# Optimization experiments

Measured on AMD Instinct MI355X. Metric: run time of the kernel, lower is better.

## Reference

```python
import jax, jax.numpy as jnp
import numpy as np

B, T, D, H = 4, 1024, 256, 4
DK = D // H


def setup_inputs() -> dict:
    key = jax.random.key(0)
    ks = jax.random.split(key, 5)
    scale = 1.0 / np.sqrt(D)
    return {
        "x": jax.random.normal(ks[0], (B, T, D), dtype=jnp.float32),
        "Wqkv": jax.random.normal(ks[1], (3 * D, D), dtype=jnp.float32) * scale,
        "bqkv": jax.random.normal(ks[2], (3 * D,), dtype=jnp.float32) * 0.01,
        "Wproj": jax.random.normal(ks[3], (D, D), dtype=jnp.float32) * scale,
        "bproj": jax.random.normal(ks[4], (D,), dtype=jnp.float32) * 0.01,
    }


def reference(x, Wqkv, bqkv, Wproj, bproj):
    # ---- temporal multi-head self-attention over T ----
    qkv = x @ Wqkv.T + bqkv                      # (B,T,3D)
    q, k, v = jnp.split(qkv, 3, axis=-1)         # each (B,T,D)
    def split_heads(t):
        return t.reshape(B, T, H, DK).transpose(0, 2, 1, 3)  # (B,H,T,DK)
    q, k, v = split_heads(q), split_heads(k), split_heads(v)
    scores_t = jnp.einsum('bhtd,bhsd->bhts', q, k) / jnp.sqrt(jnp.float32(DK))
    w_t = jax.nn.softmax(scores_t, axis=-1)       # (B,H,T,T)
    ctx = jnp.einsum('bhts,bhsd->bhtd', w_t, v)   # (B,H,T,DK)
    ctx = ctx.transpose(0, 2, 1, 3).reshape(B, T, D)
    y_t = ctx @ Wproj.T + bproj                   # (B,T,D)

    # ---- spatial (feature-pairwise) attention per timestep ----
    scores_f = jnp.einsum('bti,btj->btij', x, x) / jnp.sqrt(jnp.float32(D))  # (B,T,F,F)
    w_f = jax.nn.softmax(scores_f, axis=-1)
    y_f = jnp.einsum('btij,btj->bti', w_f, x)     # (B,T,D)

    # serial mode: y = y_t + y_f
    return y_t + y_f
```

## Files before the change

kernel.cpp:

```cpp
#include <hip/hip_runtime.h>
#include <hip/hip_bf16.h>


typedef __attribute__((ext_vector_type(8))) short short8;
typedef __attribute__((ext_vector_type(4))) float f32x4;

__device__ __forceinline__ short f2bf(float f) {
    __hip_bfloat16 h = __float2bfloat16(f);
    return __builtin_bit_cast(short, h);
}
__device__ __forceinline__ float b2f(short s) {
    unsigned u = ((unsigned)(unsigned short)s) << 16;
    return __builtin_bit_cast(float, u);
}
__device__ __forceinline__ short8 pack8(float4 a, float4 b) {
    return (short8){ f2bf(a.x), f2bf(a.y), f2bf(a.z), f2bf(a.w),
                     f2bf(b.x), f2bf(b.y), f2bf(b.z), f2bf(b.w) };
}

#if __has_builtin(__builtin_amdgcn_exp2f)
__device__ __forceinline__ float fast_exp2(float f) { return __builtin_amdgcn_exp2f(f); }
#else
__device__ __forceinline__ float fast_exp2(float f) { return exp2f(f); }
#endif

__global__ __launch_bounds__(256) void k_qkv_sp(
    const float* __restrict__ x,
    const float* __restrict__ wq,
    const float* __restrict__ bqkv,
    short* __restrict__ qkvb,
    short* __restrict__ vT,
    float* __restrict__ yf)
{
    const int bx = blockIdx.x;
    const int tid = threadIdx.x;

    if (bx >= 768) {
        const int w = tid >> 6, lane = tid & 63;
        const int row = (bx - 768)*4 + w;
        const float* xr = &x[(size_t)row*256];
        float xj[4], u[4];
        #pragma unroll
        for (int q = 0; q < 4; ++q) { xj[q] = xr[lane + q*64]; u[q] = xj[q] * 0.25f; }
        float S[16];
        float t0 = 1.f, t1 = 1.f, t2 = 1.f, t3 = 1.f;
        #pragma unroll
        for (int k = 0; k < 16; ++k) {
            S[k] = (t0 + t1) + (t2 + t3);
            if (k < 15) { t0 *= u[0]; t1 *= u[1]; t2 *= u[2]; t3 *= u[3]; }
        }
        #pragma unroll
        for (int k = 0; k < 16; ++k) {
            #pragma unroll
            for (int off = 32; off >= 1; off >>= 1)
                S[k] += __shfl_xor(S[k], off);
        }
        const float invfact[16] = {
            1.f, 1.f, 0.5f, 1.f/6, 1.f/24, 1.f/120, 1.f/720, 1.f/5040,
            1.f/40320, 1.f/362880, 1.f/3628800, 1.f/39916800, 1.f/479001600,
            1.f/6227020800.f, 1.f/87178291200.f, 1.f/1307674368000.f };
        float a[16], bcf[15];
        #pragma unroll
        for (int k = 0; k < 16; ++k) a[k] = S[k] * invfact[k];
        #pragma unroll
        for (int k = 0; k < 15; ++k) bcf[k] = 4.f * S[k+1] * invfact[k];
        float* yr = &yf[(size_t)row*256];
        #pragma unroll
        for (int q = 0; q < 4; ++q) {
            float v = u[q];
            float den = a[15];
            #pragma unroll
            for (int k = 14; k >= 0; --k) den = fmaf(den, v, a[k]);
            float num = bcf[14];
            #pragma unroll
            for (int k = 13; k >= 0; --k) num = fmaf(num, v, bcf[k]);
            yr[lane + q*64] = num / den;
        }
        return;
    }

    __shared__ __attribute__((aligned(16))) short As[64*64];
    __shared__ __attribute__((aligned(16))) short Bs[64*64];
    const int bn = bx >> 6, bm = bx & 63;
    const int w = tid >> 6, lane = tid & 63, ln = lane & 15, quad = lane >> 4;
    const int r0 = tid >> 3, c0 = (tid & 7) * 8;

    float4 xa0, xa1, xb0, xb1, wa0, wa1, wb0, wb1;
#define LOADT(K0) { \
    const float* pa0 = &x[(size_t)(bm*64 + r0)*256 + (K0) + c0]; \
    xa0 = *(const float4*)pa0; xa1 = *(const float4*)(pa0 + 4); \
    const float* pa1 = &x[(size_t)(bm*64 + r0 + 32)*256 + (K0) + c0]; \
    xb0 = *(const float4*)pa1; xb1 = *(const float4*)(pa1 + 4); \
    const float* pw0 = &wq[(size_t)(bn*64 + r0)*256 + (K0) + c0]; \
    wa0 = *(const float4*)pw0; wa1 = *(const float4*)(pw0 + 4); \
    const float* pw1 = &wq[(size_t)(bn*64 + r0 + 32)*256 + (K0) + c0]; \
    wb0 = *(const float4*)pw1; wb1 = *(const float4*)(pw1 + 4); }

    f32x4 acc[4];
    #pragma unroll
    for (int i = 0; i < 4; ++i) acc[i] = (f32x4){0.f,0.f,0.f,0.f};

    LOADT(0);
    for (int k0 = 0; k0 < 256; k0 += 64) {
        *(short8*)&As[r0*64 + c0]      = pack8(xa0, xa1);
        *(short8*)&As[(r0+32)*64 + c0] = pack8(xb0, xb1);
        *(short8*)&Bs[r0*64 + c0]      = pack8(wa0, wa1);
        *(short8*)&Bs[(r0+32)*64 + c0] = pack8(wb0, wb1);
        __syncthreads();
        if (k0 < 192) LOADT(k0 + 64);
        #pragma unroll
        for (int ks = 0; ks < 2; ++ks) {
            short8 bf = *(const short8*)&Bs[(w*16 + ln)*64 + ks*32 + quad*8];
            #pragma unroll
            for (int mt = 0; mt < 4; ++mt) {
                short8 af = *(const short8*)&As[(mt*16 + ln)*64 + ks*32 + quad*8];
                acc[mt] = __builtin_amdgcn_mfma_f32_16x16x32_bf16(af, bf, acc[mt], 0, 0, 0);
            }
        }
        if (k0 < 192) __syncthreads();
    }
#undef LOADT
    const int n = bn*64 + w*16 + ln;
    const float bias = bqkv[n];
    #pragma unroll
    for (int mt = 0; mt < 4; ++mt) {
        #pragma unroll
        for (int r = 0; r < 4; ++r) {
            int m = bm*64 + mt*16 + quad*4 + r;
            float v = acc[mt][r] + bias;
            if (bn < 8) qkvb[(size_t)m*512 + n] = f2bf(v);
            else        vT[(size_t)(n - 512)*4096 + m] = f2bf(v);
        }
    }
}

__global__ __launch_bounds__(256) void k_attn(
    const short* __restrict__ qkvb,
    const short* __restrict__ vT,
    short* __restrict__ opart,
    float* __restrict__ lpart)
{
    __shared__ __attribute__((aligned(16))) char smem[27648];
    short* Ks = (short*)smem;
    short* Vs = (short*)(smem + 9216);
    short* Ps = (short*)(smem + 18432);
    const int bx = blockIdx.x;
    const int tid = threadIdx.x;
    const int w = tid >> 6, lane = tid & 63;
    const int qb = bx >> 2, quarter = bx & 3;
    const int h = blockIdx.y, b = blockIdx.z;
    const int ln = lane & 15, quad = lane >> 4;
    const int qg = b*1024 + qb*64 + w*16 + ln;
    const float SC = 0.18033688f;

    short8 qf[2];
    #pragma unroll
    for (int ks = 0; ks < 2; ++ks)
        qf[ks] = *(const short8*)&qkvb[(size_t)qg*512 + h*64 + ks*32 + quad*8];

    const int sr0 = tid >> 3, sc0 = (tid & 7) * 8;
    const int sr1 = sr0 + 32;
    short8 kreg[2], vreg[2];
#define LOADC(CH) { \
    kreg[0] = *(const short8*)&qkvb[(size_t)(b*1024 + (CH)*64 + sr0)*512 + 256 + h*64 + sc0]; \
    vreg[0] = *(const short8*)&vT[(size_t)(h*64 + sr0)*4096 + b*1024 + (CH)*64 + sc0]; \
    kreg[1] = *(const short8*)&qkvb[(size_t)(b*1024 + (CH)*64 + sr1)*512 + 256 + h*64 + sc0]; \
    vreg[1] = *(const short8*)&vT[(size_t)(h*64 + sr1)*4096 + b*1024 + (CH)*64 + sc0]; }

    f32x4 O[4];
    #pragma unroll
    for (int i = 0; i < 4; ++i) O[i] = (f32x4){0.f,0.f,0.f,0.f};
    float lrow[4] = {0.f, 0.f, 0.f, 0.f};

    const int cbase = quarter*4;
    LOADC(cbase);
    for (int kc = 0; kc < 4; ++kc) {
        __syncthreads();
        *(short8*)&Ks[sr0*72 + sc0] = kreg[0];
        *(short8*)&Vs[sr0*72 + sc0] = vreg[0];
        *(short8*)&Ks[sr1*72 + sc0] = kreg[1];
        *(short8*)&Vs[sr1*72 + sc0] = vreg[1];
        __syncthreads();
        if (kc < 3) LOADC(cbase + kc + 1);

        f32x4 s[4];
        #pragma unroll
        for (int nt = 0; nt < 4; ++nt) {
            s[nt] = (f32x4){0.f,0.f,0.f,0.f};
            #pragma unroll
            for (int ks = 0; ks < 2; ++ks) {
                short8 kf = *(const short8*)&Ks[(nt*16 + ln)*72 + ks*32 + quad*8];
                s[nt] = __builtin_amdgcn_mfma_f32_16x16x32_bf16(qf[ks], kf, s[nt], 0, 0, 0);
            }
        }
        #pragma unroll
        for (int nt = 0; nt < 4; ++nt) {
            #pragma unroll
            for (int r = 0; r < 4; ++r) {
                float e = fast_exp2(s[nt][r] * SC);
                lrow[r] += e;
                Ps[w*1152 + (quad*4 + r)*72 + nt*16 + ln] = f2bf(e);
            }
        }
        short8 pf[2];
        #pragma unroll
        for (int ks = 0; ks < 2; ++ks)
            pf[ks] = *(const short8*)&Ps[w*1152 + ln*72 + ks*32 + quad*8];

        #pragma unroll
        for (int dt = 0; dt < 4; ++dt) {
            #pragma unroll
            for (int ks = 0; ks < 2; ++ks) {
                short8 vf = *(const short8*)&Vs[(dt*16 + ln)*72 + ks*32 + quad*8];
                O[dt] = __builtin_amdgcn_mfma_f32_16x16x32_bf16(pf[ks], vf, O[dt], 0, 0, 0);
            }
        }
    }
#undef LOADC

    short* op = opart + (size_t)quarter * (4096*256);
    #pragma unroll
    for (int r = 0; r < 4; ++r) {
        int rowi = quad*4 + r;
        float l = lrow[r];
        #pragma unroll
        for (int off = 8; off >= 1; off >>= 1) l += __shfl_xor(l, off);
        int m = b*1024 + qb*64 + w*16 + rowi;
        if (ln == 0) lpart[(size_t)quarter*16384 + m*4 + h] = l;
        #pragma unroll
        for (int dt = 0; dt < 4; ++dt)
            op[(size_t)m*256 + h*64 + dt*16 + ln] = f2bf(O[dt][r]);
    }
}

__global__ __launch_bounds__(256) void k_proj(
    const short* __restrict__ opart,
    const float* __restrict__ lpart,
    const float* __restrict__ wp,
    const float* __restrict__ bproj,
    const float* __restrict__ yf,
    float* __restrict__ out)
{
    __shared__ __attribute__((aligned(16))) short As[64*64];
    __shared__ __attribute__((aligned(16))) short Bs[64*64];
    const int bn = blockIdx.x, bm = blockIdx.y;
    const int tid = threadIdx.x;
    const int w = tid >> 6, lane = tid & 63, ln = lane & 15, quad = lane >> 4;
    const int r0 = tid >> 3, c0 = (tid & 7) * 8;
    const size_t OP = (size_t)4096*256;

    short8 amix0, amix1;
    float4 wa0, wa1, wb0, wb1;
#define LOADT(K0) { \
    const int hh = (K0) >> 6; \
    const int m0 = bm*64 + r0, m1 = bm*64 + r0 + 32; \
    float il0 = 1.0f / (lpart[m0*4 + hh] + lpart[16384 + m0*4 + hh] + \
                        lpart[32768 + m0*4 + hh] + lpart[49152 + m0*4 + hh]); \
    float il1 = 1.0f / (lpart[m1*4 + hh] + lpart[16384 + m1*4 + hh] + \
                        lpart[32768 + m1*4 + hh] + lpart[49152 + m1*4 + hh]); \
    short8 a0 = *(const short8*)&opart[(size_t)m0*256 + (K0) + c0]; \
    short8 a1 = *(const short8*)&opart[OP + (size_t)m0*256 + (K0) + c0]; \
    short8 a2 = *(const short8*)&opart[2*OP + (size_t)m0*256 + (K0) + c0]; \
    short8 a3 = *(const short8*)&opart[3*OP + (size_t)m0*256 + (K0) + c0]; \
    short8 b0 = *(const short8*)&opart[(size_t)m1*256 + (K0) + c0]; \
    short8 b1 = *(const short8*)&opart[OP + (size_t)m1*256 + (K0) + c0]; \
    short8 b2 = *(const short8*)&opart[2*OP + (size_t)m1*256 + (K0) + c0]; \
    short8 b3 = *(const short8*)&opart[3*OP + (size_t)m1*256 + (K0) + c0]; \
    _Pragma("unroll") \
    for (int e = 0; e < 8; ++e) { \
        amix0[e] = f2bf(((b2f(a0[e]) + b2f(a1[e])) + (b2f(a2[e]) + b2f(a3[e]))) * il0); \
        amix1[e] = f2bf(((b2f(b0[e]) + b2f(b1[e])) + (b2f(b2[e]) + b2f(b3[e]))) * il1); \
    } \
    const float* pw0 = &wp[(size_t)(bn*64 + r0)*256 + (K0) + c0]; \
    wa0 = *(const float4*)pw0; wa1 = *(const float4*)(pw0 + 4); \
    const float* pw1 = &wp[(size_t)(bn*64 + r0 + 32)*256 + (K0) + c0]; \
    wb0 = *(const float4*)pw1; wb1 = *(const float4*)(pw1 + 4); }

    f32x4 acc[4];
    #pragma unroll
    for (int i = 0; i < 4; ++i) acc[i] = (f32x4){0.f,0.f,0.f,0.f};

    LOADT(0);
    for (int k0 = 0; k0 < 256; k0 += 64) {
        *(short8*)&As[r0*64 + c0]      = amix0;
        *(short8*)&As[(r0+32)*64 + c0] = amix1;
        *(short8*)&Bs[r0*64 + c0]      = pack8(wa0, wa1);
        *(short8*)&Bs[(r0+32)*64 + c0] = pack8(wb0, wb1);
        __syncthreads();
        if (k0 < 192) LOADT(k0 + 64);
        #pragma unroll
        for (int ks = 0; ks < 2; ++ks) {
            short8 bf = *(const short8*)&Bs[(w*16 + ln)*64 + ks*32 + quad*8];
            #pragma unroll
            for (int mt = 0; mt < 4; ++mt) {
                short8 af = *(const short8*)&As[(mt*16 + ln)*64 + ks*32 + quad*8];
                acc[mt] = __builtin_amdgcn_mfma_f32_16x16x32_bf16(af, bf, acc[mt], 0, 0, 0);
            }
        }
        if (k0 < 192) __syncthreads();
    }
#undef LOADT
    const int n = bn*64 + w*16 + ln;
    const float bias = bproj[n];
    #pragma unroll
    for (int mt = 0; mt < 4; ++mt) {
        #pragma unroll
        for (int r = 0; r < 4; ++r) {
            int m = bm*64 + mt*16 + quad*4 + r;
            out[(size_t)m*256 + n] = acc[mt][r] + bias + yf[(size_t)m*256 + n];
        }
    }
}

extern "C" void kernel_launch(void* const* d_in, const int* in_sizes, int n_in,
                              void* d_out, int out_size, void* d_ws, size_t ws_size,
                              hipStream_t stream) {
    const float* x     = (const float*)d_in[0];
    const float* Wqkv  = (const float*)d_in[1];
    const float* bqkv  = (const float*)d_in[2];
    const float* Wproj = (const float*)d_in[3];
    const float* bproj = (const float*)d_in[4];
    float* out = (float*)d_out;

    short* qkvb  = (short*)d_ws;
    short* vTb   = qkvb + 2097152;
    short* opart = vTb + 1048576;
    float* lpart = (float*)(opart + 4*1048576);
    float* yf    = lpart + 4*16384;

    k_qkv_sp<<<dim3(768 + 1024), 256, 0, stream>>>(x, Wqkv, bqkv, qkvb, vTb, yf);
    k_attn<<<dim3(64, 4, 4), 256, 0, stream>>>(qkvb, vTb, opart, lpart);
    k_proj<<<dim3(4, 64), 256, 0, stream>>>(opart, lpart, Wproj, bproj, yf, out);
}
```

Before: 102.1 us.

## Switch attention to 32x32 MFMA with register-resident P and atomic row sums

```diff
diff --git a/kernel.cpp b/kernel.cpp
--- a/kernel.cpp
+++ b/kernel.cpp
@@ -4,6 +4,8 @@
 
 typedef __attribute__((ext_vector_type(8))) short short8;
 typedef __attribute__((ext_vector_type(4))) float f32x4;
+typedef __attribute__((ext_vector_type(16))) float f32x16;
+typedef __attribute__((ext_vector_type(4))) unsigned u32x4;
 
 __device__ __forceinline__ short f2bf(float f) {
     __hip_bfloat16 h = __float2bfloat16(f);
@@ -16,6 +18,11 @@
 __device__ __forceinline__ short8 pack8(float4 a, float4 b) {
     return (short8){ f2bf(a.x), f2bf(a.y), f2bf(a.z), f2bf(a.w),
                      f2bf(b.x), f2bf(b.y), f2bf(b.z), f2bf(b.w) };
+}
+__device__ __forceinline__ unsigned pack2bf(float lo, float hi) {
+    unsigned ul = (unsigned)(unsigned short)f2bf(lo);
+    unsigned uh = (unsigned)(unsigned short)f2bf(hi);
+    return ul | (uh << 16);
 }
 
 #if __has_builtin(__builtin_amdgcn_exp2f)
@@ -30,14 +37,17 @@
     const float* __restrict__ bqkv,
     short* __restrict__ qkvb,
     short* __restrict__ vT,
-    float* __restrict__ yf)
+    float* __restrict__ yf,
+    float* __restrict__ lsum)
 {
     const int bx = blockIdx.x;
     const int tid = threadIdx.x;
 
     if (bx >= 768) {
+        const int sb = bx - 768;
+        if (sb < 64) lsum[sb*256 + tid] = 0.f;
         const int w = tid >> 6, lane = tid & 63;
-        const int row = (bx - 768)*4 + w;
+        const int row = sb*4 + w;
         const float* xr = &x[(size_t)row*256];
         float xj[4], u[4];
         #pragma unroll
@@ -79,8 +89,9 @@
         return;
     }
 
-    __shared__ __attribute__((aligned(16))) short As[64*64];
-    __shared__ __attribute__((aligned(16))) short Bs[64*64];
+    __shared__ __attribute__((aligned(16))) short sAB[8192];
+    short* As = sAB;
+    short* Bs = sAB + 4096;
     const int bn = bx >> 6, bm = bx & 63;
     const int w = tid >> 6, lane = tid & 63, ln = lane & 15, quad = lane >> 4;
     const int r0 = tid >> 3, c0 = (tid & 7) * 8;
@@ -122,15 +133,32 @@
 #undef LOADT
     const int n = bn*64 + w*16 + ln;
     const float bias = bqkv[n];
-    #pragma unroll
-    for (int mt = 0; mt < 4; ++mt) {
-        #pragma unroll
-        for (int r = 0; r < 4; ++r) {
-            int m = bm*64 + mt*16 + quad*4 + r;
-            float v = acc[mt][r] + bias;
-            if (bn < 8) qkvb[(size_t)m*512 + n] = f2bf(v);
-            else        vT[(size_t)(n - 512)*4096 + m] = f2bf(v);
-        }
+    if (bn < 8) {
+        #pragma unroll
+        for (int mt = 0; mt < 4; ++mt) {
+            #pragma unroll
+            for (int r = 0; r < 4; ++r) {
+                int m = bm*64 + mt*16 + quad*4 + r;
+                qkvb[(size_t)m*512 + n] = f2bf(acc[mt][r] + bias);
+            }
+        }
+    } else {
+        __syncthreads();
+        short* Ts = sAB;
+        #pragma unroll
+        for (int mt = 0; mt < 4; ++mt) {
+            #pragma unroll
+            for (int r = 0; r < 4; ++r)
+                Ts[(w*16 + ln)*72 + mt*16 + quad*4 + r] = f2bf(acc[mt][r] + bias);
+        }
+        __syncthreads();
+        const int rw = tid >> 2;
+        const int cc = (tid & 3) * 16;
+        short8 t0 = *(const short8*)&Ts[rw*72 + cc];
+        short8 t1 = *(const short8*)&Ts[rw*72 + cc + 8];
+        short* dst = &vT[(size_t)((bn - 8)*64 + rw)*4096 + bm*64 + cc];
+        *(short8*)dst       = t0;
+        *(short8*)(dst + 8) = t1;
     }
 }
 
@@ -138,25 +166,22 @@
     const short* __restrict__ qkvb,
     const short* __restrict__ vT,
     short* __restrict__ opart,
-    float* __restrict__ lpart)
+    float* __restrict__ lsum)
 {
-    __shared__ __attribute__((aligned(16))) char smem[27648];
-    short* Ks = (short*)smem;
-    short* Vs = (short*)(smem + 9216);
-    short* Ps = (short*)(smem + 18432);
-    const int bx = blockIdx.x;
+    __shared__ __attribute__((aligned(16))) short Ks[64*72];
+    __shared__ __attribute__((aligned(16))) short Vs[64*72];
     const int tid = threadIdx.x;
     const int w = tid >> 6, lane = tid & 63;
-    const int qb = bx >> 2, quarter = bx & 3;
+    const int l31 = lane & 31, h2 = lane >> 5;
+    const int qb = blockIdx.x >> 2, quarter = blockIdx.x & 3;
     const int h = blockIdx.y, b = blockIdx.z;
-    const int ln = lane & 15, quad = lane >> 4;
-    const int qg = b*1024 + qb*64 + w*16 + ln;
     const float SC = 0.18033688f;
 
-    short8 qf[2];
-    #pragma unroll
-    for (int ks = 0; ks < 2; ++ks)
-        qf[ks] = *(const short8*)&qkvb[(size_t)qg*512 + h*64 + ks*32 + quad*8];
+    const int qrow = b*1024 + qb*128 + w*32 + l31;
+    short8 qf[4];
+    #pragma unroll
+    for (int ks = 0; ks < 4; ++ks)
+        qf[ks] = *(const short8*)&qkvb[(size_t)qrow*512 + h*64 + ks*16 + h2*8];
 
     const int sr0 = tid >> 3, sc0 = (tid & 7) * 8;
     const int sr1 = sr0 + 32;
@@ -167,10 +192,10 @@
     kreg[1] = *(const short8*)&qkvb[(size_t)(b*1024 + (CH)*64 + sr1)*512 + 256 + h*64 + sc0]; \
     vreg[1] = *(const short8*)&vT[(size_t)(h*64 + sr1)*4096 + b*1024 + (CH)*64 + sc0]; }
 
-    f32x4 O[4];
-    #pragma unroll
-    for (int i = 0; i < 4; ++i) O[i] = (f32x4){0.f,0.f,0.f,0.f};
-    float lrow[4] = {0.f, 0.f, 0.f, 0.f};
+    f32x16 O0, O1;
+    #pragma unroll
+    for (int i = 0; i < 16; ++i) { O0[i] = 0.f; O1[i] = 0.f; }
+    float lrow = 0.f;
 
     const int cbase = quarter*4;
     LOADC(cbase);
@@ -183,59 +208,71 @@
         __syncthreads();
         if (kc < 3) LOADC(cbase + kc + 1);
 
-        f32x4 s[4];
-        #pragma unroll
-        for (int nt = 0; nt < 4; ++nt) {
-            s[nt] = (f32x4){0.f,0.f,0.f,0.f};
-            #pragma unroll
-            for (int ks = 0; ks < 2; ++ks) {
-                short8 kf = *(const short8*)&Ks[(nt*16 + ln)*72 + ks*32 + quad*8];
-                s[nt] = __builtin_amdgcn_mfma_f32_16x16x32_bf16(qf[ks], kf, s[nt], 0, 0, 0);
-            }
-        }
-        #pragma unroll
-        for (int nt = 0; nt < 4; ++nt) {
-            #pragma unroll
-            for (int r = 0; r < 4; ++r) {
-                float e = fast_exp2(s[nt][r] * SC);
-                lrow[r] += e;
-                Ps[w*1152 + (quad*4 + r)*72 + nt*16 + ln] = f2bf(e);
-            }
-        }
-        short8 pf[2];
-        #pragma unroll
-        for (int ks = 0; ks < 2; ++ks)
-            pf[ks] = *(const short8*)&Ps[w*1152 + ln*72 + ks*32 + quad*8];
-
-        #pragma unroll
-        for (int dt = 0; dt < 4; ++dt) {
-            #pragma unroll
-            for (int ks = 0; ks < 2; ++ks) {
-                short8 vf = *(const short8*)&Vs[(dt*16 + ln)*72 + ks*32 + quad*8];
-                O[dt] = __builtin_amdgcn_mfma_f32_16x16x32_bf16(pf[ks], vf, O[dt], 0, 0, 0);
+        f32x16 s0, s1;
+        #pragma unroll
+        for (int i = 0; i < 16; ++i) { s0[i] = 0.f; s1[i] = 0.f; }
+        #pragma unroll
+        for (int ks = 0; ks < 4; ++ks) {
+            short8 kf0 = *(const short8*)&Ks[l31*72 + ks*16 + h2*8];
+            s0 = __builtin_amdgcn_mfma_f32_32x32x16_bf16(kf0, qf[ks], s0, 0, 0, 0);
+            short8 kf1 = *(const short8*)&Ks[(32 + l31)*72 + ks*16 + h2*8];
+            s1 = __builtin_amdgcn_mfma_f32_32x32x16_bf16(kf1, qf[ks], s1, 0, 0, 0);
+        }
+
+        short8 pa[2][2];
+        #pragma unroll
+        for (int kb = 0; kb < 2; ++kb) {
+            const f32x16& sv = kb ? s1 : s0;
+            float e[16];
+            #pragma unroll
+            for (int r = 0; r < 16; ++r) {
+                e[r] = fast_exp2(sv[r] * SC);
+                lrow += e[r];
+            }
+            unsigned c[8];
+            #pragma unroll
+            for (int p = 0; p < 8; ++p) c[p] = pack2bf(e[2*p], e[2*p+1]);
+            #pragma unroll
+            for (int ks2 = 0; ks2 < 2; ++ks2) {
+                unsigned w0 = c[4*ks2 + 0], w2 = c[4*ks2 + 2];
+                unsigned w1 = c[4*ks2 + 1], w3 = c[4*ks2 + 3];
+                asm("v_permlane32_swap_b32 %0, %1" : "+v"(w0), "+v"(w2));
+                asm("v_permlane32_swap_b32 %0, %1" : "+v"(w1), "+v"(w3));
+                u32x4 pw = (u32x4){w0, w1, w2, w3};
+                pa[kb][ks2] = __builtin_bit_cast(short8, pw);
+            }
+        }
+
+        #pragma unroll
+        for (int dt = 0; dt < 2; ++dt) {
+            f32x16& Od = dt ? O1 : O0;
+            #pragma unroll
+            for (int kb = 0; kb < 2; ++kb) {
+                #pragma unroll
+                for (int ks2 = 0; ks2 < 2; ++ks2) {
+                    short8 vf = *(const short8*)&Vs[(dt*32 + l31)*72 + kb*32 + ks2*16 + h2*8];
+                    Od = __builtin_amdgcn_mfma_f32_32x32x16_bf16(pa[kb][ks2], vf, Od, 0, 0, 0);
+                }
             }
         }
     }
 #undef LOADC
 
+    lrow += __shfl_xor(lrow, 32);
+    if (lane < 32) atomicAdd(&lsum[qrow*4 + h], lrow);
+
     short* op = opart + (size_t)quarter * (4096*256);
     #pragma unroll
-    for (int r = 0; r < 4; ++r) {
-        int rowi = quad*4 + r;
-        float l = lrow[r];
-        #pragma unroll
-        for (int off = 8; off >= 1; off >>= 1) l += __shfl_xor(l, off);
-        int m = b*1024 + qb*64 + w*16 + rowi;
-        if (ln == 0) lpart[(size_t)quarter*16384 + m*4 + h] = l;
-        #pragma unroll
-        for (int dt = 0; dt < 4; ++dt)
-            op[(size_t)m*256 + h*64 + dt*16 + ln] = f2bf(O[dt][r]);
+    for (int reg = 0; reg < 16; ++reg) {
+        int qr = b*1024 + qb*128 + w*32 + (reg & 3) + 8*(reg >> 2) + 4*h2;
+        op[(size_t)qr*256 + h*64 + l31]      = f2bf(O0[reg]);
+        op[(size_t)qr*256 + h*64 + 32 + l31] = f2bf(O1[reg]);
     }
 }
 
 __global__ __launch_bounds__(256) void k_proj(
     const short* __restrict__ opart,
-    const float* __restrict__ lpart,
+    const float* __restrict__ lsum,
     const float* __restrict__ wp,
     const float* __restrict__ bproj,
     const float* __restrict__ yf,
@@ -254,10 +291,8 @@
 #define LOADT(K0) { \
     const int hh = (K0) >> 6; \
     const int m0 = bm*64 + r0, m1 = bm*64 + r0 + 32; \
-    float il0 = 1.0f / (lpart[m0*4 + hh] + lpart[16384 + m0*4 + hh] + \
-                        lpart[32768 + m0*4 + hh] + lpart[49152 + m0*4 + hh]); \
-    float il1 = 1.0f / (lpart[m1*4 + hh] + lpart[16384 + m1*4 + hh] + \
-                        lpart[32768 + m1*4 + hh] + lpart[49152 + m1*4 + hh]); \
+    float il0 = 1.0f / lsum[m0*4 + hh]; \
+    float il1 = 1.0f / lsum[m1*4 + hh]; \
     short8 a0 = *(const short8*)&opart[(size_t)m0*256 + (K0) + c0]; \
     short8 a1 = *(const short8*)&opart[OP + (size_t)m0*256 + (K0) + c0]; \
     short8 a2 = *(const short8*)&opart[2*OP + (size_t)m0*256 + (K0) + c0]; \
@@ -325,10 +360,10 @@
     short* qkvb  = (short*)d_ws;
     short* vTb   = qkvb + 2097152;
     short* opart = vTb + 1048576;
-    float* lpart = (float*)(opart + 4*1048576);
-    float* yf    = lpart + 4*16384;
-
-    k_qkv_sp<<<dim3(768 + 1024), 256, 0, stream>>>(x, Wqkv, bqkv, qkvb, vTb, yf);
-    k_attn<<<dim3(64, 4, 4), 256, 0, stream>>>(qkvb, vTb, opart, lpart);
-    k_proj<<<dim3(4, 64), 256, 0, stream>>>(opart, lpart, Wproj, bproj, yf, out);
-}
+    float* lsum  = (float*)(opart + 4*1048576);
+    float* yf    = lsum + 16384;
+
+    k_qkv_sp<<<dim3(768 + 1024), 256, 0, stream>>>(x, Wqkv, bqkv, qkvb, vTb, yf, lsum);
+    k_attn<<<dim3(32, 4, 4), 256, 0, stream>>>(qkvb, vTb, opart, lsum);
+    k_proj<<<dim3(4, 64), 256, 0, stream>>>(opart, lsum, Wproj, bproj, yf, out);
+}
```

Measured after the change: 95.89 us. 6.1% less time.
